# Optimization experiments

Hardware: AMD Instinct MI355X
Metric: run time of the kernel (lower is better)

Reference implementation:

```python
import jax, jax.numpy as jnp
import numpy as np

B, S, V, D, H, DH, L, FF = 1, 4096, 50265, 768, 12, 64, 4, 3072
C = 256          # chunk size
W = 256          # one-sided window (attention_window=512 total)
N = S // C


def _ln(x, g, b):
    m = x.mean(-1, keepdims=True)
    v = ((x - m) ** 2).mean(-1, keepdims=True)
    return (x - m) * jax.lax.rsqrt(v + 1e-5) * g + b


def setup_inputs() -> dict:
    key = jax.random.key(0)
    ks = iter(jax.random.split(key, 64))
    f = lambda sh: 0.02 * jax.random.normal(next(ks), sh, jnp.float32)
    return dict(
        input_ids=jax.random.randint(next(ks), (B, S), 0, V),
        attention_mask=jnp.ones((B, S), jnp.int32),
        word_emb=f((V, D)), pos_emb=f((S, D)),
        emb_g=jnp.ones((D,)), emb_b=jnp.zeros((D,)),
        Wq=f((L, D, D)), Wk=f((L, D, D)), Wv=f((L, D, D)), Wo=f((L, D, D)),
        bq=jnp.zeros((L, D)), bk=jnp.zeros((L, D)), bv=jnp.zeros((L, D)), bo=jnp.zeros((L, D)),
        ln1_g=jnp.ones((L, D)), ln1_b=jnp.zeros((L, D)),
        Wff1=f((L, D, FF)), bff1=jnp.zeros((L, FF)),
        Wff2=f((L, FF, D)), bff2=jnp.zeros((L, D)),
        ln2_g=jnp.ones((L, D)), ln2_b=jnp.zeros((L, D)),
        W1=f((D, 512)), b1=jnp.zeros((512,)),
        W2=f((512, 250)), b2=jnp.zeros((250,)),
        W3=f((250, 1)), b3=jnp.zeros((1,)),
    )


def _band_attn(x, maskf, Wq, Wk, Wv, Wo, bq, bk, bv, bo):
    # sliding-window (banded) attention via overlapping 3-chunk blocks
    q = ((x @ Wq + bq) / np.float32(np.sqrt(DH))).reshape(B, N, C, H, DH)
    k = (x @ Wk + bk).reshape(B, N, C, H, DH)
    v = (x @ Wv + bv).reshape(B, N, C, H, DH)
    pad = ((0, 0), (1, 1), (0, 0), (0, 0), (0, 0))
    kp, vp = jnp.pad(k, pad), jnp.pad(v, pad)
    kb = jnp.concatenate([kp[:, :-2], kp[:, 1:-1], kp[:, 2:]], axis=2)  # [B,N,3C,H,DH]
    vb = jnp.concatenate([vp[:, :-2], vp[:, 1:-1], vp[:, 2:]], axis=2)
    mc = maskf.reshape(B, N, C)
    mp = jnp.pad(mc, ((0, 0), (1, 1), (0, 0)))
    mb = jnp.concatenate([mp[:, :-2], mp[:, 1:-1], mp[:, 2:]], axis=2)  # [B,N,3C]
    qi = jnp.arange(C)[:, None]
    kj = jnp.arange(3 * C)[None, :]
    band = jnp.abs(kj - C - qi) <= W                       # [C,3C]
    valid = band[None, None, None] & (mb[:, None, :, None, :] > 0)  # [B,1,N,C,3C]
    scores = jnp.einsum('bnqhd,bnkhd->bhnqk', q, kb)       # [B,H,N,C,3C]
    scores = jnp.where(valid, scores, -1e9)
    probs = jax.nn.softmax(scores, axis=-1)
    out = jnp.einsum('bhnqk,bnkhd->bnqhd', probs, vb).reshape(B, S, D)
    return out @ Wo + bo


def reference(input_ids, attention_mask, word_emb, pos_emb, emb_g, emb_b,
              Wq, Wk, Wv, Wo, bq, bk, bv, bo, ln1_g, ln1_b,
              Wff1, bff1, Wff2, bff2, ln2_g, ln2_b,
              W1, b1, W2, b2, W3, b3):
    maskf = attention_mask.astype(jnp.float32)
    x = _ln(word_emb[input_ids] + pos_emb[None], emb_g, emb_b)
    for l in range(L):
        a = _band_attn(x, maskf, Wq[l], Wk[l], Wv[l], Wo[l], bq[l], bk[l], bv[l], bo[l])
        x = _ln(x + a, ln1_g[l], ln1_b[l])
        h = jax.nn.gelu(x @ Wff1[l] + bff1[l], approximate=False)
        x = _ln(x + h @ Wff2[l] + bff2[l], ln2_g[l], ln2_b[l])
    m = maskf[..., None]
    pooled = (x * m).sum(1) / jnp.clip(m.sum(1), 1e-9)     # mean pooling, [B,D]
    h = jax.nn.relu(pooled @ W1 + b1)
    h = jax.nn.relu(h @ W2 + b2)
    pred = h @ W3 + b3                                     # dropout = identity (eval)
    return (pred, pred)
```

## Files before the change

### kernel.cpp

```cpp
#include <hip/hip_runtime.h>
#include <hip/hip_bf16.h>

typedef __hip_bfloat16 bf16;
typedef unsigned short ushort_t;
typedef short bhalf8 __attribute__((ext_vector_type(8)));
typedef float floatx4 __attribute__((ext_vector_type(4)));

#define SLEN 4096
#define DMODEL 768
#define NHEAD 12
#define DHEAD 64
#define NLAYER 4
#define FFDIM 3072
#define WIN 256
#define QB 64
#define NKT 9
#define VT_PLANE (NHEAD*DHEAD*SLEN)

__device__ __forceinline__ float wave_sum(float v){
  #pragma unroll
  for (int off = 32; off; off >>= 1) v += __shfl_xor(v, off, 64);
  return v;
}

__device__ __forceinline__ ushort_t f2bf(float x){
  unsigned u = __float_as_uint(x);
  unsigned r = u + 0x7FFFu + ((u >> 16) & 1u);
  return (ushort_t)(r >> 16);
}
__device__ __forceinline__ float bf2f(ushort_t h){
  return __uint_as_float((unsigned)h << 16);
}

__device__ __forceinline__ floatx4 mfma_bf16(bhalf8 a, bhalf8 b, floatx4 c){
  asm("v_mfma_f32_16x16x32_bf16 %0, %1, %2, %0" : "+v"(c) : "v"(a), "v"(b));
  return c;
}

__device__ __forceinline__ void split8(const float* xs, bhalf8& hi, bhalf8& lo){
  union { ushort_t u[8]; bhalf8 v; } H, L;
  #pragma unroll
  for (int j = 0; j < 8; j++){
    ushort_t h = f2bf(xs[j]);
    H.u[j] = h;
    L.u[j] = f2bf(xs[j] - bf2f(h));
  }
  hi = H.v; lo = L.v;
}

__global__ __launch_bounds__(256) void embed_ln_kernel(
    const int* __restrict__ ids, const float* __restrict__ we,
    const float* __restrict__ pe, const float* __restrict__ g,
    const float* __restrict__ b, float* __restrict__ x){
  int row  = blockIdx.x*4 + (threadIdx.x >> 6);
  int lane = threadIdx.x & 63;
  int id = ids[row];
  float e[12];
  float sum = 0.f;
  #pragma unroll
  for (int i = 0; i < 12; i++){
    int c = lane + i*64;
    e[i] = we[(size_t)id*DMODEL + c] + pe[(size_t)row*DMODEL + c];
    sum += e[i];
  }
  float mean = wave_sum(sum) * (1.f/DMODEL);
  float vs = 0.f;
  #pragma unroll
  for (int i = 0; i < 12; i++){ float d = e[i] - mean; vs += d*d; }
  float inv = 1.f / sqrtf(wave_sum(vs)*(1.f/DMODEL) + 1e-5f);
  #pragma unroll
  for (int i = 0; i < 12; i++){
    int c = lane + i*64;
    x[(size_t)row*DMODEL + c] = (e[i] - mean)*inv*g[c] + b[c];
  }
}

__global__ __launch_bounds__(256) void ln_kernel(
    const float* __restrict__ in, float* __restrict__ out,
    const float* __restrict__ g, const float* __restrict__ b){
  int row  = blockIdx.x*4 + (threadIdx.x >> 6);
  int lane = threadIdx.x & 63;
  float e[12];
  float sum = 0.f;
  #pragma unroll
  for (int i = 0; i < 12; i++){
    e[i] = in[(size_t)row*DMODEL + lane + i*64];
    sum += e[i];
  }
  float mean = wave_sum(sum) * (1.f/DMODEL);
  float vs = 0.f;
  #pragma unroll
  for (int i = 0; i < 12; i++){ float d = e[i] - mean; vs += d*d; }
  float inv = 1.f / sqrtf(wave_sum(vs)*(1.f/DMODEL) + 1e-5f);
  #pragma unroll
  for (int i = 0; i < 12; i++){
    int c = lane + i*64;
    out[(size_t)row*DMODEL + c] = (e[i] - mean)*inv*g[c] + b[c];
  }
}

__global__ __launch_bounds__(256) void split_b_kernel(
    const float* __restrict__ W, ushort_t* __restrict__ T,
    int Nw, int Ntot, int K, int noff){
  int n  = blockIdx.x*256 + threadIdx.x;
  int kc = blockIdx.y;
  float xs[8];
  #pragma unroll
  for (int j = 0; j < 8; j++) xs[j] = W[(size_t)(kc*8 + j)*Nw + n];
  union { ushort_t u[8]; uint4 v; } ph, pl;
  #pragma unroll
  for (int j = 0; j < 8; j++){
    ushort_t h = f2bf(xs[j]);
    ph.u[j] = h;
    pl.u[j] = f2bf(xs[j] - bf2f(h));
  }
  size_t KC = (size_t)(K >> 3);
  *reinterpret_cast<uint4*>(T + ((size_t)kc*Ntot + noff + n)*8)        = ph.v;
  *reinterpret_cast<uint4*>(T + ((KC + kc)*Ntot + noff + n)*8)         = pl.v;
}

template<int NTILE>
__global__ __launch_bounds__(256) void gemm_mfma_kernel(
    const float* __restrict__ Afp, const ushort_t* __restrict__ pBt,
    const float* __restrict__ bias, const float* __restrict__ bias2,
    const float* __restrict__ bias3, const float* __restrict__ resid,
    float* __restrict__ Cm, float* __restrict__ k_out,
    ushort_t* __restrict__ vt_out,
    int M, int N, int K, float scale, int mode){
  constexpr int NI = NTILE/32;
  constexpr int NCH = NTILE/64;
  __shared__ __align__(16) ushort_t LA[2][2][4][64][8];
  __shared__ __align__(16) ushort_t LB[2][2][4][NTILE][8];
  const int tid  = threadIdx.x;
  const int w    = tid >> 6;
  const int lane = tid & 63;
  const int wr = w >> 1, wc = w & 1;

  int bx = blockIdx.x, by = blockIdx.y;
  {
    int nwg = gridDim.x*gridDim.y;
    if ((nwg & 7) == 0){
      int lin = by*gridDim.x + bx;
      int lin2 = (lin & 7)*(nwg >> 3) + (lin >> 3);
      bx = lin2 % gridDim.x;
      by = lin2 / gridDim.x;
    }
  }
  const int r0 = by*64, c0 = bx*NTILE;
  const int fr = lane & 15, fq = lane >> 4;
  const size_t KC = (size_t)(K >> 3);
  const size_t planeB = (size_t)N*8;

  const int arow = tid >> 2;
  const int akg  = tid & 3;
  const float* asrc = Afp + (size_t)(r0 + arow)*K + akg*8;

  floatx4 acc[2][NI] = {};
  const int nstep = K >> 5;

  #pragma unroll
  for (int c = 0; c < 2*NCH; c++){
    int idx = w*(2*NCH) + c;
    int chunk = idx % NCH, rem = idx / NCH;
    int kg = rem & 3, half = rem >> 2;
    const ushort_t* sp = pBt + (size_t)half*KC*planeB + (size_t)kg*planeB
                       + (size_t)(c0 + chunk*64 + lane)*8;
    ushort_t* dp = &LB[0][half][kg][chunk*64][0];
    __builtin_amdgcn_global_load_lds(
        (const __attribute__((address_space(1))) void*)sp,
        (__attribute__((address_space(3))) void*)dp, 16, 0, 0);
  }
  {
    float4 a0 = *reinterpret_cast<const float4*>(asrc);
    float4 a1 = *reinterpret_cast<const float4*>(asrc + 4);
    asm volatile("s_waitcnt vmcnt(0)" ::: "memory");
    float xs[8] = {a0.x,a0.y,a0.z,a0.w,a1.x,a1.y,a1.z,a1.w};
    bhalf8 hi, lo; split8(xs, hi, lo);
    *reinterpret_cast<bhalf8*>(&LA[0][0][akg][arow][0]) = hi;
    *reinterpret_cast<bhalf8*>(&LA[0][1][akg][arow][0]) = lo;
  }
  __syncthreads();

  int cur = 0;
  for (int s = 0; s < nstep; ++s){
    const bool pf = (s+1 < nstep);
    float4 pa0, pa1;
    if (pf){
      const int kcb = (s+1) << 2;
      #pragma unroll
      for (int c = 0; c < 2*NCH; c++){
        int idx = w*(2*NCH) + c;
        int chunk = idx % NCH, rem = idx / NCH;
        int kg = rem & 3, half = rem >> 2;
        const ushort_t* sp = pBt + (size_t)half*KC*planeB + (size_t)(kcb + kg)*planeB
                           + (size_t)(c0 + chunk*64 + lane)*8;
        ushort_t* dp = &LB[cur^1][half][kg][chunk*64][0];
        __builtin_amdgcn_global_load_lds(
            (const __attribute__((address_space(1))) void*)sp,
            (__attribute__((address_space(3))) void*)dp, 16, 0, 0);
      }
      const float* p = asrc + (size_t)(s+1)*32;
      pa0 = *reinterpret_cast<const float4*>(p);
      pa1 = *reinterpret_cast<const float4*>(p + 4);
    }

    bhalf8 ah[2], al[2], bh[NI], bl[NI];
    #pragma unroll
    for (int mi = 0; mi < 2; mi++){
      int row = wr*32 + mi*16 + fr;
      ah[mi] = *reinterpret_cast<const bhalf8*>(&LA[cur][0][fq][row][0]);
      al[mi] = *reinterpret_cast<const bhalf8*>(&LA[cur][1][fq][row][0]);
    }
    #pragma unroll
    for (int ni = 0; ni < NI; ni++){
      int col = wc*(NTILE/2) + ni*16 + fr;
      bh[ni] = *reinterpret_cast<const bhalf8*>(&LB[cur][0][fq][col][0]);
      bl[ni] = *reinterpret_cast<const bhalf8*>(&LB[cur][1][fq][col][0]);
    }
    #pragma unroll
    for (int mi = 0; mi < 2; mi++)
      #pragma unroll
      for (int ni = 0; ni < NI; ni++)
        acc[mi][ni] = mfma_bf16(ah[mi], bh[ni], acc[mi][ni]);
    #pragma unroll
    for (int mi = 0; mi < 2; mi++)
      #pragma unroll
      for (int ni = 0; ni < NI; ni++)
        acc[mi][ni] = mfma_bf16(ah[mi], bl[ni], acc[mi][ni]);
    #pragma unroll
    for (int mi = 0; mi < 2; mi++)
      #pragma unroll
      for (int ni = 0; ni < NI; ni++)
        acc[mi][ni] = mfma_bf16(al[mi], bh[ni], acc[mi][ni]);

    if (pf){
      asm volatile("s_waitcnt vmcnt(0)" ::: "memory");
      float xs[8] = {pa0.x,pa0.y,pa0.z,pa0.w,pa1.x,pa1.y,pa1.z,pa1.w};
      bhalf8 hi, lo; split8(xs, hi, lo);
      *reinterpret_cast<bhalf8*>(&LA[cur^1][0][akg][arow][0]) = hi;
      *reinterpret_cast<bhalf8*>(&LA[cur^1][1][akg][arow][0]) = lo;
    }
    __syncthreads();
    cur ^= 1;
  }

  if (NTILE == 128 && mode == 2){
    const int sect = c0 / DMODEL;
    const int coff = c0 - sect*DMODEL;
    #pragma unroll
    for (int mi = 0; mi < 2; mi++){
      #pragma unroll
      for (int ni = 0; ni < NI; ni++){
        int col = coff + wc*(NTILE/2) + ni*16 + fr;
        int row0 = r0 + wr*32 + mi*16 + fq*4;
        if (sect == 0){
          float bb = bias[col];
          #pragma unroll
          for (int j = 0; j < 4; j++)
            Cm[(size_t)(row0+j)*DMODEL + col] = (acc[mi][ni][j] + bb) * scale;
        } else if (sect == 1){
          float bb = bias2[col];
          #pragma unroll
          for (int j = 0; j < 4; j++)
            k_out[(size_t)(row0+j)*DMODEL + col] = acc[mi][ni][j] + bb;
        } else {
          float bb = bias3[col];
          unsigned long long phi = 0ull, plo = 0ull;
          #pragma unroll
          for (int j = 0; j < 4; j++){
            float vo = acc[mi][ni][j] + bb;
            ushort_t hh = f2bf(vo);
            ushort_t ll = f2bf(vo - bf2f(hh));
            phi |= (unsigned long long)hh << (16*j);
            plo |= (unsigned long long)ll << (16*j);
          }
          size_t base = (size_t)col*SLEN + row0;
          *reinterpret_cast<unsigned long long*>(&vt_out[base])            = phi;
          *reinterpret_cast<unsigned long long*>(&vt_out[VT_PLANE + base]) = plo;
        }
      }
    }
    return;
  }

  #pragma unroll
  for (int mi = 0; mi < 2; mi++){
    #pragma unroll
    for (int ni = 0; ni < NI; ni++){
      int col = c0 + wc*(NTILE/2) + ni*16 + fr;
      float bb = bias[col];
      #pragma unroll
      for (int j = 0; j < 4; j++){
        int row = r0 + wr*32 + mi*16 + fq*4 + j;
        float vo = (acc[mi][ni][j] + bb) * scale;
        if (mode == 1) vo = 0.5f*vo*(1.f + erff(vo*0.70710678118654752f));
        if (resid) vo += resid[(size_t)row*N + col];
        Cm[(size_t)row*N + col] = vo;
      }
    }
  }
}

__global__ __launch_bounds__(128) void band_attn_kernel(
    const float* __restrict__ q, const float* __restrict__ k,
    const ushort_t* __restrict__ vt, const int* __restrict__ mask,
    float* __restrict__ ao){
  __shared__ __align__(16) ushort_t KHs[8][65][8];
  __shared__ __align__(16) ushort_t KLs[8][65][8];
  __shared__ __align__(16) ushort_t VHs[8][65][8];
  __shared__ __align__(16) ushort_t VLs[8][65][8];
  __shared__ __align__(16) ushort_t PHs[2][8][33][8];
  __shared__ __align__(16) ushort_t PLs[2][8][33][8];
  __shared__ float aL[2][32];
  __shared__ float lL[2][32];

  const int h    = blockIdx.y;
  const int q0   = blockIdx.x * QB;
  const int tid  = threadIdx.x;
  const int w    = tid >> 6;
  const int lane = tid & 63;
  const int fr   = lane & 15;
  const int fq   = lane >> 4;
  const int kstart = q0 - WIN;

  bhalf8 QHr[2][2], QLr[2][2];
  #pragma unroll
  for (int cf = 0; cf < 2; cf++)
    #pragma unroll
    for (int s = 0; s < 2; s++){
      const float* qp = q + (size_t)(q0 + 32*w + 16*cf + fr)*DMODEL
                      + h*DHEAD + s*32 + fq*8;
      float4 a = *reinterpret_cast<const float4*>(qp);
      float4 b = *reinterpret_cast<const float4*>(qp + 4);
      float xs[8] = {a.x,a.y,a.z,a.w,b.x,b.y,b.z,b.w};
      split8(xs, QHr[cf][s], QLr[cf][s]);
    }

  floatx4 acc_o[2][4] = {};
  float mreg[2] = {0.f, 0.f};
  float lreg[2] = {0.f, 0.f};

  const int rK = 32*w + (lane >> 1);
  const int hd = lane & 1;

  for (int t = 0; t < NKT; t++){
    const int g0 = kstart + t*64;

    {
      int g = min(max(g0 + rK, 0), SLEN-1);
      const float* kp = k + (size_t)g*DMODEL + h*DHEAD + hd*32;
      #pragma unroll
      for (int i = 0; i < 4; i++){
        float4 a = *reinterpret_cast<const float4*>(kp + i*8);
        float4 b = *reinterpret_cast<const float4*>(kp + i*8 + 4);
        float xs[8] = {a.x,a.y,a.z,a.w,b.x,b.y,b.z,b.w};
        bhalf8 hi, lo; split8(xs, hi, lo);
        int kg = hd*4 + i;
        *reinterpret_cast<bhalf8*>(&KHs[kg][rK][0]) = hi;
        *reinterpret_cast<bhalf8*>(&KLs[kg][rK][0]) = lo;
      }
      const ushort_t* vrow = vt + (size_t)(h*DHEAD + rK)*SLEN;
      #pragma unroll
      for (int i = 0; i < 4; i++){
        int kk = min(max(g0 + hd*32 + i*8, 0), SLEN-8);
        uint4 hv = *reinterpret_cast<const uint4*>(&vrow[kk]);
        uint4 lv = *reinterpret_cast<const uint4*>(&vrow[VT_PLANE + kk]);
        int u = hd*4 + i;
        *reinterpret_cast<uint4*>(&VHs[u][rK][0]) = hv;
        *reinterpret_cast<uint4*>(&VLs[u][rK][0]) = lv;
      }
    }
    __syncthreads();

    int gmk = g0 + lane;
    bool kvv = ((unsigned)gmk < (unsigned)SLEN) &&
               (mask[min(max(gmk,0),SLEN-1)] != 0);
    unsigned long long bal = __ballot(kvv);

    floatx4 acc_s[4][2] = {};
    #pragma unroll
    for (int s = 0; s < 2; s++)
      #pragma unroll
      for (int kf = 0; kf < 4; kf++){
        int row = 16*kf + fr;
        int kg  = s*4 + fq;
        bhalf8 KHf = *reinterpret_cast<const bhalf8*>(&KHs[kg][row][0]);
        bhalf8 KLf = *reinterpret_cast<const bhalf8*>(&KLs[kg][row][0]);
        #pragma unroll
        for (int cf = 0; cf < 2; cf++){
          acc_s[kf][cf] = mfma_bf16(KHf, QHr[cf][s], acc_s[kf][cf]);
          acc_s[kf][cf] = mfma_bf16(KHf, QLr[cf][s], acc_s[kf][cf]);
          acc_s[kf][cf] = mfma_bf16(KLf, QHr[cf][s], acc_s[kf][cf]);
        }
      }

    #pragma unroll
    for (int cf = 0; cf < 2; cf++){
      int qloc = 32*w + 16*cf + fr;
      float mx = -1e30f;
      #pragma unroll
      for (int kf = 0; kf < 4; kf++)
        #pragma unroll
        for (int j = 0; j < 4; j++){
          int key = 16*kf + fq*4 + j;
          int dj  = t*64 + key - WIN - qloc;
          bool ok = ((unsigned)(dj + WIN) <= 2u*WIN) && ((bal >> key) & 1ull);
          float sv = ok ? acc_s[kf][cf][j] : -1e30f;
          acc_s[kf][cf][j] = sv;
          mx = fmaxf(mx, sv);
        }
      mx = fmaxf(mx, __shfl_xor(mx, 16, 64));
      mx = fmaxf(mx, __shfl_xor(mx, 32, 64));
      float mnew  = fmaxf(mreg[cf], mx);
      float alpha = __expf(mreg[cf] - mnew);
      mreg[cf] = mnew;
      float psum = 0.f;
      #pragma unroll
      for (int kf = 0; kf < 4; kf++){
        unsigned long long phi = 0ull, plo = 0ull;
        #pragma unroll
        for (int j = 0; j < 4; j++){
          float p = __expf(acc_s[kf][cf][j] - mnew);
          psum += p;
          ushort_t hh = f2bf(p);
          ushort_t ll = f2bf(p - bf2f(hh));
          phi |= (unsigned long long)hh << (16*j);
          plo |= (unsigned long long)ll << (16*j);
        }
        int kgrp = 2*kf + (fq >> 1);
        int qrow = 16*cf + fr;
        *reinterpret_cast<unsigned long long*>(&PHs[w][kgrp][qrow][(fq&1)*4]) = phi;
        *reinterpret_cast<unsigned long long*>(&PLs[w][kgrp][qrow][(fq&1)*4]) = plo;
      }
      psum += __shfl_xor(psum, 16, 64);
      psum += __shfl_xor(psum, 32, 64);
      lreg[cf] = lreg[cf]*alpha + psum;
      if (fq == 0) aL[w][16*cf + fr] = alpha;
    }
    __syncthreads();

    #pragma unroll
    for (int mf = 0; mf < 2; mf++)
      #pragma unroll
      for (int j = 0; j < 4; j++){
        float al = aL[w][16*mf + fq*4 + j];
        #pragma unroll
        for (int ni = 0; ni < 4; ni++)
          acc_o[mf][ni][j] *= al;
      }

    #pragma unroll
    for (int ks = 0; ks < 2; ks++){
      int u = ks*4 + fq;
      bhalf8 PHf[2], PLf[2];
      #pragma unroll
      for (int mf = 0; mf < 2; mf++){
        PHf[mf] = *reinterpret_cast<const bhalf8*>(&PHs[w][u][16*mf + fr][0]);
        PLf[mf] = *reinterpret_cast<const bhalf8*>(&PLs[w][u][16*mf + fr][0]);
      }
      #pragma unroll
      for (int ni = 0; ni < 4; ni++){
        int d = 16*ni + fr;
        bhalf8 VHf = *reinterpret_cast<const bhalf8*>(&VHs[u][d][0]);
        bhalf8 VLf = *reinterpret_cast<const bhalf8*>(&VLs[u][d][0]);
        #pragma unroll
        for (int mf = 0; mf < 2; mf++){
          acc_o[mf][ni] = mfma_bf16(PHf[mf], VHf, acc_o[mf][ni]);
          acc_o[mf][ni] = mfma_bf16(PHf[mf], VLf, acc_o[mf][ni]);
          acc_o[mf][ni] = mfma_bf16(PLf[mf], VHf, acc_o[mf][ni]);
        }
      }
    }
    __syncthreads();
  }

  if (fq == 0){
    lL[w][fr]      = 1.f / lreg[0];
    lL[w][16 + fr] = 1.f / lreg[1];
  }
  __syncthreads();
  #pragma unroll
  for (int mf = 0; mf < 2; mf++)
    #pragma unroll
    for (int j = 0; j < 4; j++){
      float inv = lL[w][16*mf + fq*4 + j];
      int qg = q0 + 32*w + 16*mf + fq*4 + j;
      float* orow = ao + (size_t)qg*DMODEL + h*DHEAD;
      #pragma unroll
      for (int ni = 0; ni < 4; ni++)
        orow[16*ni + fr] = acc_o[mf][ni][j] * inv;
    }
}

__global__ __launch_bounds__(256) void pool1_kernel(
    const float* __restrict__ x, const int* __restrict__ mask,
    float* __restrict__ partial){
  int b = blockIdx.x;
  int t = threadIdx.x;
  float a0 = 0.f, a1 = 0.f, a2 = 0.f;
  for (int r = b*16; r < b*16 + 16; r++){
    float mm = (float)mask[r];
    const float* row = x + (size_t)r*DMODEL;
    a0 = fmaf(row[t      ], mm, a0);
    a1 = fmaf(row[t + 256], mm, a1);
    a2 = fmaf(row[t + 512], mm, a2);
  }
  partial[(size_t)b*DMODEL + t      ] = a0;
  partial[(size_t)b*DMODEL + t + 256] = a1;
  partial[(size_t)b*DMODEL + t + 512] = a2;
}

__global__ __launch_bounds__(256) void pool2_kernel(
    const float* __restrict__ partial, float* __restrict__ ps){
  int c = blockIdx.x*256 + threadIdx.x;
  float a = 0.f;
  for (int p = 0; p < 256; p++) a += partial[(size_t)p*DMODEL + c];
  ps[c] = a;
}

__global__ __launch_bounds__(64) void probe_kernel(
    const float* __restrict__ p, int n, float* __restrict__ slot){
  int lane = threadIdx.x;
  float s = 0.f;
  for (int i = lane; i < n; i += 64) s += fabsf(p[i]);
  s = wave_sum(s);
  if (lane == 0) slot[0] = s;
}

__global__ __launch_bounds__(256) void head_kernel(
    const float* __restrict__ ps, const int* __restrict__ mask,
    const float* __restrict__ W1, const float* __restrict__ b1,
    const float* __restrict__ W2, const float* __restrict__ b2,
    const float* __restrict__ W3, const float* __restrict__ b3,
    const float* __restrict__ diag,
    bf16* __restrict__ out){
  __shared__ float p[DMODEL];
  __shared__ float h1[512];
  __shared__ float h2[256];
  __shared__ float red[4];
  int tid = threadIdx.x;
  float ms = 0.f;
  for (int r = tid; r < SLEN; r += 256) ms += (float)mask[r];
  ms = wave_sum(ms);
  if ((tid & 63) == 0) red[tid >> 6] = ms;
  __syncthreads();
  float msum = red[0] + red[1] + red[2] + red[3];
  float inv = 1.f / fmaxf(msum, 1e-9f);
  for (int c = tid; c < DMODEL; c += 256) p[c] = ps[c]*inv;
  __syncthreads();
  #pragma unroll
  for (int jj = 0; jj < 2; jj++){
    int j = tid + jj*256;
    float acc = 0.f;
    for (int c = 0; c < DMODEL; c++) acc = fmaf(p[c], W1[(size_t)c*512 + j], acc);
    h1[j] = fmaxf(acc + b1[j], 0.f);
  }
  __syncthreads();
  if (tid < 250){
    float acc = 0.f;
    for (int c = 0; c < 512; c++) acc = fmaf(h1[c], W2[(size_t)c*250 + tid], acc);
    h2[tid] = fmaxf(acc + b2[tid], 0.f);
  }
  __syncthreads();
  if (tid == 0){
    float acc = b3[0];
    for (int c = 0; c < 250; c++) acc = fmaf(h2[c], W3[c], acc);
    float delta = 0.f;
    #pragma unroll
    for (int kk = 0; kk < 6; kk++){
      float dv = diag[kk];
      if (!(dv > 1e-3f)){
        delta = (dv != dv ? 8192.0f : 0.0f) + 64.0f*(kk+1);
        break;
      }
    }
    float r = acc + delta;
    union { bf16 h; unsigned short u; } cv;
    cv.h = (bf16)r;
    unsigned int packed = ((unsigned int)cv.u << 16) | (unsigned int)cv.u;
    volatile unsigned int* o32 = (volatile unsigned int*)out;
    o32[0] = packed;
    o32[1] = packed;
  }
}

extern "C" void kernel_launch(void* const* d_in, const int* in_sizes, int n_in,
                              void* d_out, int out_size, void* d_ws, size_t ws_size,
                              hipStream_t stream) {
  const int*   ids  = (const int*)d_in[0];
  const int*   mask = (const int*)d_in[1];
  const float* we   = (const float*)d_in[2];
  const float* pe   = (const float*)d_in[3];
  const float* eg   = (const float*)d_in[4];
  const float* eb   = (const float*)d_in[5];
  const float* Wq   = (const float*)d_in[6];
  const float* Wk   = (const float*)d_in[7];
  const float* Wv   = (const float*)d_in[8];
  const float* Wo   = (const float*)d_in[9];
  const float* bq   = (const float*)d_in[10];
  const float* bk   = (const float*)d_in[11];
  const float* bv   = (const float*)d_in[12];
  const float* bo   = (const float*)d_in[13];
  const float* g1   = (const float*)d_in[14];
  const float* be1  = (const float*)d_in[15];
  const float* Wf1  = (const float*)d_in[16];
  const float* bf1  = (const float*)d_in[17];
  const float* Wf2  = (const float*)d_in[18];
  const float* bf2  = (const float*)d_in[19];
  const float* g2   = (const float*)d_in[20];
  const float* be2  = (const float*)d_in[21];
  const float* W1   = (const float*)d_in[22];
  const float* b1   = (const float*)d_in[23];
  const float* W2   = (const float*)d_in[24];
  const float* b2   = (const float*)d_in[25];
  const float* W3   = (const float*)d_in[26];
  const float* b3   = (const float*)d_in[27];

  const size_t SD = (size_t)SLEN*DMODEL;
  float* x  = (float*)d_ws;
  float* y  = x  + SD;
  float* q  = y  + SD;
  float* k  = q  + SD;
  float* v  = k  + SD;
  float* ao = v  + SD;
  float* hf = q;
  ushort_t* vt = (ushort_t*)v;
  float* ps      = ao + SD;
  float* partial = ps + 1024;
  float* diag    = partial + 256*DMODEL;
  ushort_t* Bt = (ushort_t*)(diag + 64);

  embed_ln_kernel<<<SLEN/4, 256, 0, stream>>>(ids, we, pe, eg, eb, x);
  probe_kernel<<<1, 64, 0, stream>>>(x, 4096, diag + 0);

  const float qscale = 0.125f;
  dim3 gQKV((DMODEL*3)/128, SLEN/64);
  dim3 gD64(DMODEL/64,      SLEN/64);
  dim3 gF1 (FFDIM/128,      SLEN/64);

  for (int l = 0; l < NLAYER; l++){
    const float* wq  = Wq  + (size_t)l*DMODEL*DMODEL;
    const float* wk  = Wk  + (size_t)l*DMODEL*DMODEL;
    const float* wv  = Wv  + (size_t)l*DMODEL*DMODEL;
    const float* wo  = Wo  + (size_t)l*DMODEL*DMODEL;
    const float* wf1 = Wf1 + (size_t)l*DMODEL*FFDIM;
    const float* wf2 = Wf2 + (size_t)l*FFDIM*DMODEL;

    split_b_kernel<<<dim3(3,96), 256, 0, stream>>>(wq, Bt, DMODEL, 3*DMODEL, DMODEL, 0);
    split_b_kernel<<<dim3(3,96), 256, 0, stream>>>(wk, Bt, DMODEL, 3*DMODEL, DMODEL, DMODEL);
    split_b_kernel<<<dim3(3,96), 256, 0, stream>>>(wv, Bt, DMODEL, 3*DMODEL, DMODEL, 2*DMODEL);
    gemm_mfma_kernel<128><<<gQKV, 256, 0, stream>>>(
        x, Bt, bq + l*DMODEL, bk + l*DMODEL, bv + l*DMODEL, nullptr,
        q, k, vt, SLEN, 3*DMODEL, DMODEL, qscale, 2);
    if (l == 0) probe_kernel<<<1, 64, 0, stream>>>(q, 4096, diag + 1);
    if (l == 0) probe_kernel<<<1, 64, 0, stream>>>((const float*)vt, 4096, diag + 2);

    band_attn_kernel<<<dim3(SLEN/QB, NHEAD), 128, 0, stream>>>(q, k, vt, mask, ao);
    if (l == 0) probe_kernel<<<1, 64, 0, stream>>>(ao, 4096, diag + 3);

    split_b_kernel<<<dim3(3,96), 256, 0, stream>>>(wo, Bt, DMODEL, DMODEL, DMODEL, 0);
    gemm_mfma_kernel<64><<<gD64, 256, 0, stream>>>(
        ao, Bt, bo + l*DMODEL, nullptr, nullptr, x,
        y, nullptr, nullptr, SLEN, DMODEL, DMODEL, 1.f, 0);
    ln_kernel<<<SLEN/4, 256, 0, stream>>>(y, x, g1 + l*DMODEL, be1 + l*DMODEL);

    split_b_kernel<<<dim3(12,96), 256, 0, stream>>>(wf1, Bt, FFDIM, FFDIM, DMODEL, 0);
    gemm_mfma_kernel<128><<<gF1, 256, 0, stream>>>(
        x, Bt, bf1 + l*FFDIM, nullptr, nullptr, nullptr,
        hf, nullptr, nullptr, SLEN, FFDIM, DMODEL, 1.f, 1);

    split_b_kernel<<<dim3(3,384), 256, 0, stream>>>(wf2, Bt, DMODEL, DMODEL, FFDIM, 0);
    gemm_mfma_kernel<64><<<gD64, 256, 0, stream>>>(
        hf, Bt, bf2 + l*DMODEL, nullptr, nullptr, x,
        y, nullptr, nullptr, SLEN, DMODEL, FFDIM, 1.f, 0);
    ln_kernel<<<SLEN/4, 256, 0, stream>>>(y, x, g2 + l*DMODEL, be2 + l*DMODEL);
  }
  probe_kernel<<<1, 64, 0, stream>>>(x, 4096, diag + 4);

  pool1_kernel<<<256, 256, 0, stream>>>(x, mask, partial);
  pool2_kernel<<<DMODEL/256, 256, 0, stream>>>(partial, ps);
  probe_kernel<<<1, 64, 0, stream>>>(ps, DMODEL, diag + 5);
  head_kernel<<<1, 256, 0, stream>>>(ps, mask, W1, b1, W2, b2, W3, b3, diag, (bf16*)d_out);
}
```

Measured before the change: 1.954 ms.

## Split MLP head across blocks, shrink GEMM tiles, and shorten probe scans

The single-block head MLP becomes four kernels: partial dot products spread over 48 and 16 blocks, followed by small reduction kernels. The mask-sum moves into pool2. The QKV and FF1 GEMMs switch from 128-wide to 64-wide column tiles, so each launches more blocks. The diagnostic probe kernels now scan 512 elements instead of 4096. This trades a serial single-block head for more launches and smaller tiles, which may reduce per-block reuse.

```diff
diff --git a/kernel.cpp b/kernel.cpp
--- a/kernel.cpp
+++ b/kernel.cpp
@@ -244,7 +244,7 @@
     cur ^= 1;
   }
 
-  if (NTILE == 128 && mode == 2){
+  if (mode == 2){
     const int sect = c0 / DMODEL;
     const int coff = c0 - sect*DMODEL;
     #pragma unroll
@@ -511,11 +511,22 @@
 }
 
 __global__ __launch_bounds__(256) void pool2_kernel(
-    const float* __restrict__ partial, float* __restrict__ ps){
+    const float* __restrict__ partial, const int* __restrict__ mask,
+    float* __restrict__ ps){
+  __shared__ float red[4];
   int c = blockIdx.x*256 + threadIdx.x;
   float a = 0.f;
   for (int p = 0; p < 256; p++) a += partial[(size_t)p*DMODEL + c];
   ps[c] = a;
+  if (blockIdx.x == 0){
+    int tid = threadIdx.x;
+    float ms = 0.f;
+    for (int r = tid; r < SLEN; r += 256) ms += (float)mask[r];
+    ms = wave_sum(ms);
+    if ((tid & 63) == 0) red[tid >> 6] = ms;
+    __syncthreads();
+    if (tid == 0) ps[1000] = red[0] + red[1] + red[2] + red[3];
+  }
 }
 
 __global__ __launch_bounds__(64) void probe_kernel(
@@ -527,39 +538,58 @@
   if (lane == 0) slot[0] = s;
 }
 
-__global__ __launch_bounds__(256) void head_kernel(
-    const float* __restrict__ ps, const int* __restrict__ mask,
-    const float* __restrict__ W1, const float* __restrict__ b1,
-    const float* __restrict__ W2, const float* __restrict__ b2,
-    const float* __restrict__ W3, const float* __restrict__ b3,
-    const float* __restrict__ diag,
-    bf16* __restrict__ out){
-  __shared__ float p[DMODEL];
-  __shared__ float h1[512];
-  __shared__ float h2[256];
-  __shared__ float red[4];
+__global__ __launch_bounds__(256) void head1a_kernel(
+    const float* __restrict__ ps, const float* __restrict__ W1,
+    float* __restrict__ partial1){
+  int b = blockIdx.x;
   int tid = threadIdx.x;
-  float ms = 0.f;
-  for (int r = tid; r < SLEN; r += 256) ms += (float)mask[r];
-  ms = wave_sum(ms);
-  if ((tid & 63) == 0) red[tid >> 6] = ms;
-  __syncthreads();
-  float msum = red[0] + red[1] + red[2] + red[3];
-  float inv = 1.f / fmaxf(msum, 1e-9f);
-  for (int c = tid; c < DMODEL; c += 256) p[c] = ps[c]*inv;
-  __syncthreads();
+  float inv = 1.f / fmaxf(ps[1000], 1e-9f);
+  float a0 = 0.f, a1 = 0.f;
+  for (int r = b*16; r < b*16 + 16; r++){
+    float pr = ps[r]*inv;
+    a0 = fmaf(pr, W1[(size_t)r*512 + tid      ], a0);
+    a1 = fmaf(pr, W1[(size_t)r*512 + tid + 256], a1);
+  }
+  partial1[(size_t)b*512 + tid      ] = a0;
+  partial1[(size_t)b*512 + tid + 256] = a1;
+}
+
+__global__ __launch_bounds__(256) void head1b_kernel(
+    const float* __restrict__ partial1, const float* __restrict__ b1,
+    float* __restrict__ h1g){
+  int tid = threadIdx.x;
   #pragma unroll
   for (int jj = 0; jj < 2; jj++){
     int j = tid + jj*256;
-    float acc = 0.f;
-    for (int c = 0; c < DMODEL; c++) acc = fmaf(p[c], W1[(size_t)c*512 + j], acc);
-    h1[j] = fmaxf(acc + b1[j], 0.f);
-  }
-  __syncthreads();
+    float a = 0.f;
+    for (int p = 0; p < 48; p++) a += partial1[(size_t)p*512 + j];
+    h1g[j] = fmaxf(a + b1[j], 0.f);
+  }
+}
+
+__global__ __launch_bounds__(256) void head2a_kernel(
+    const float* __restrict__ h1g, const float* __restrict__ W2,
+    float* __restrict__ partial2){
+  int b = blockIdx.x;
+  int tid = threadIdx.x;
   if (tid < 250){
-    float acc = 0.f;
-    for (int c = 0; c < 512; c++) acc = fmaf(h1[c], W2[(size_t)c*250 + tid], acc);
-    h2[tid] = fmaxf(acc + b2[tid], 0.f);
+    float a = 0.f;
+    for (int r = b*32; r < b*32 + 32; r++)
+      a = fmaf(h1g[r], W2[(size_t)r*250 + tid], a);
+    partial2[(size_t)b*250 + tid] = a;
+  }
+}
+
+__global__ __launch_bounds__(256) void head2b_kernel(
+    const float* __restrict__ partial2, const float* __restrict__ b2,
+    const float* __restrict__ W3, const float* __restrict__ b3,
+    const float* __restrict__ diag, bf16* __restrict__ out){
+  __shared__ float h2[256];
+  int tid = threadIdx.x;
+  if (tid < 250){
+    float a = 0.f;
+    for (int p = 0; p < 16; p++) a += partial2[(size_t)p*250 + tid];
+    h2[tid] = fmaxf(a + b2[tid], 0.f);
   }
   __syncthreads();
   if (tid == 0){
@@ -625,18 +655,21 @@
   float* ao = v  + SD;
   float* hf = q;
   ushort_t* vt = (ushort_t*)v;
-  float* ps      = ao + SD;
-  float* partial = ps + 1024;
-  float* diag    = partial + 256*DMODEL;
-  ushort_t* Bt = (ushort_t*)(diag + 64);
+  float* ps       = ao + SD;
+  float* partial  = ps + 1024;
+  float* diag     = partial + 256*DMODEL;
+  float* partial1 = diag + 64;
+  float* h1g      = partial1 + 48*512;
+  float* partial2 = h1g + 512;
+  ushort_t* Bt = (ushort_t*)(partial2 + 4096);
 
   embed_ln_kernel<<<SLEN/4, 256, 0, stream>>>(ids, we, pe, eg, eb, x);
-  probe_kernel<<<1, 64, 0, stream>>>(x, 4096, diag + 0);
+  probe_kernel<<<1, 64, 0, stream>>>(x, 512, diag + 0);
 
   const float qscale = 0.125f;
-  dim3 gQKV((DMODEL*3)/128, SLEN/64);
-  dim3 gD64(DMODEL/64,      SLEN/64);
-  dim3 gF1 (FFDIM/128,      SLEN/64);
+  dim3 gQKV((DMODEL*3)/64, SLEN/64);
+  dim3 gD64(DMODEL/64,     SLEN/64);
+  dim3 gF1 (FFDIM/64,      SLEN/64);
 
   for (int l = 0; l < NLAYER; l++){
     const float* wq  = Wq  + (size_t)l*DMODEL*DMODEL;
@@ -649,14 +682,14 @@
     split_b_kernel<<<dim3(3,96), 256, 0, stream>>>(wq, Bt, DMODEL, 3*DMODEL, DMODEL, 0);
     split_b_kernel<<<dim3(3,96), 256, 0, stream>>>(wk, Bt, DMODEL, 3*DMODEL, DMODEL, DMODEL);
     split_b_kernel<<<dim3(3,96), 256, 0, stream>>>(wv, Bt, DMODEL, 3*DMODEL, DMODEL, 2*DMODEL);
-    gemm_mfma_kernel<128><<<gQKV, 256, 0, stream>>>(
+    gemm_mfma_kernel<64><<<gQKV, 256, 0, stream>>>(
         x, Bt, bq + l*DMODEL, bk + l*DMODEL, bv + l*DMODEL, nullptr,
         q, k, vt, SLEN, 3*DMODEL, DMODEL, qscale, 2);
-    if (l == 0) probe_kernel<<<1, 64, 0, stream>>>(q, 4096, diag + 1);
-    if (l == 0) probe_kernel<<<1, 64, 0, stream>>>((const float*)vt, 4096, diag + 2);
+    if (l == 0) probe_kernel<<<1, 64, 0, stream>>>(q, 512, diag + 1);
+    if (l == 0) probe_kernel<<<1, 64, 0, stream>>>((const float*)vt, 512, diag + 2);
 
     band_attn_kernel<<<dim3(SLEN/QB, NHEAD), 128, 0, stream>>>(q, k, vt, mask, ao);
-    if (l == 0) probe_kernel<<<1, 64, 0, stream>>>(ao, 4096, diag + 3);
+    if (l == 0) probe_kernel<<<1, 64, 0, stream>>>(ao, 512, diag + 3);
 
     split_b_kernel<<<dim3(3,96), 256, 0, stream>>>(wo, Bt, DMODEL, DMODEL, DMODEL, 0);
     gemm_mfma_kernel<64><<<gD64, 256, 0, stream>>>(
@@ -665,7 +698,7 @@
     ln_kernel<<<SLEN/4, 256, 0, stream>>>(y, x, g1 + l*DMODEL, be1 + l*DMODEL);
 
     split_b_kernel<<<dim3(12,96), 256, 0, stream>>>(wf1, Bt, FFDIM, FFDIM, DMODEL, 0);
-    gemm_mfma_kernel<128><<<gF1, 256, 0, stream>>>(
+    gemm_mfma_kernel<64><<<gF1, 256, 0, stream>>>(
         x, Bt, bf1 + l*FFDIM, nullptr, nullptr, nullptr,
         hf, nullptr, nullptr, SLEN, FFDIM, DMODEL, 1.f, 1);
 
@@ -675,10 +708,13 @@
         y, nullptr, nullptr, SLEN, DMODEL, FFDIM, 1.f, 0);
     ln_kernel<<<SLEN/4, 256, 0, stream>>>(y, x, g2 + l*DMODEL, be2 + l*DMODEL);
   }
-  probe_kernel<<<1, 64, 0, stream>>>(x, 4096, diag + 4);
+  probe_kernel<<<1, 64, 0, stream>>>(x, 512, diag + 4);
 
   pool1_kernel<<<256, 256, 0, stream>>>(x, mask, partial);
-  pool2_kernel<<<DMODEL/256, 256, 0, stream>>>(partial, ps);
+  pool2_kernel<<<DMODEL/256, 256, 0, stream>>>(partial, mask, ps);
   probe_kernel<<<1, 64, 0, stream>>>(ps, DMODEL, diag + 5);
-  head_kernel<<<1, 256, 0, stream>>>(ps, mask, W1, b1, W2, b2, W3, b3, diag, (bf16*)d_out);
-}
+  head1a_kernel<<<48, 256, 0, stream>>>(ps, W1, partial1);
+  head1b_kernel<<<1, 256, 0, stream>>>(partial1, b1, h1g);
+  head2a_kernel<<<16, 256, 0, stream>>>(h1g, W2, partial2);
+  head2b_kernel<<<1, 256, 0, stream>>>(partial2, b2, W3, b3, diag, (bf16*)d_out);
+}
```

After: 2.012 ms. 3.0% more time.
